# Performance work log

Hardware: AMD Instinct MI355X
Metric: run time of the kernel (lower is better)

Reference implementation:

```python
import jax, jax.numpy as jnp
import numpy as np

D_MODEL = 256
N_LAYERS = 6
PATCH = 160
N_CLASSES = 8
MAX_SEQ = 6000


def _layernorm(x, scale, bias, eps=1e-5):
    mu = jnp.mean(x, axis=-1, keepdims=True)
    var = jnp.var(x, axis=-1, keepdims=True)
    return (x - mu) * jax.lax.rsqrt(var + eps) * scale + bias


def _gru_layer(x, w_ih, w_hh, b_ih, b_hh):
    # x: [B,S,D]; w_ih,w_hh: [3D,D]; b_*: [3D]. PyTorch gate order: r,z,n.
    B, S, D = x.shape
    xp = jnp.einsum('bsd,gd->bsg', x, w_ih) + b_ih  # [B,S,3D], precompute input proj
    xp = jnp.swapaxes(xp, 0, 1)  # [S,B,3D]

    def step(h, xpt):
        gh = jnp.einsum('bd,gd->bg', h, w_hh) + b_hh
        xr, xz, xn = jnp.split(xpt, 3, axis=-1)
        hr, hz, hn = jnp.split(gh, 3, axis=-1)
        r = jax.nn.sigmoid(xr + hr)
        z = jax.nn.sigmoid(xz + hz)
        n = jnp.tanh(xn + r * hn)
        h_new = (1.0 - z) * n + z * h
        return h_new, h_new

    h0 = jnp.zeros((B, D), dtype=x.dtype)
    _, ys = jax.lax.scan(step, h0, xp)  # [S,B,D]
    return jnp.swapaxes(ys, 0, 1)


def setup_inputs() -> dict:
    key = jax.random.key(0)
    ks = jax.random.split(key, 16)
    D, L = D_MODEL, N_LAYERS
    s = lambda *sh: 0.02
    inp = {
        'waveform': jax.random.normal(ks[0], (32, 160000), dtype=jnp.float32) * 0.5,
        'conv_w': jax.random.normal(ks[1], (PATCH, D), dtype=jnp.float32) * (1.0 / np.sqrt(PATCH)),
        'pos_emb': jax.random.normal(ks[2], (MAX_SEQ, D), dtype=jnp.float32) * 0.02,
        'ln_scale': jnp.ones((L, D), dtype=jnp.float32),
        'ln_bias': jnp.zeros((L, D), dtype=jnp.float32),
        'w_ih': jax.random.normal(ks[3], (L, 3 * D, D), dtype=jnp.float32) * (1.0 / np.sqrt(D)),
        'w_hh': jax.random.normal(ks[4], (L, 3 * D, D), dtype=jnp.float32) * (1.0 / np.sqrt(D)),
        'b_ih': jnp.zeros((L, 3 * D), dtype=jnp.float32),
        'b_hh': jnp.zeros((L, 3 * D), dtype=jnp.float32),
        'fnorm_scale': jnp.ones((D,), dtype=jnp.float32),
        'fnorm_bias': jnp.zeros((D,), dtype=jnp.float32),
        'head_w1': jax.random.normal(ks[5], (D, D // 2), dtype=jnp.float32) * (1.0 / np.sqrt(D)),
        'head_b1': jnp.zeros((D // 2,), dtype=jnp.float32),
        'head_w2': jax.random.normal(ks[6], (D // 2, N_CLASSES), dtype=jnp.float32) * (1.0 / np.sqrt(D // 2)),
        'head_b2': jnp.zeros((N_CLASSES,), dtype=jnp.float32),
    }
    return inp


def reference(waveform, conv_w, pos_emb, ln_scale, ln_bias, w_ih, w_hh, b_ih, b_hh,
              fnorm_scale, fnorm_bias, head_w1, head_b1, head_w2, head_b2):
    B, T = waveform.shape
    S = T // PATCH
    # Conv1d(k=stride=PATCH, no bias) == patchify + matmul, then exact GELU
    x = waveform[:, : S * PATCH].reshape(B, S, PATCH)
    x = jax.nn.gelu(jnp.einsum('bsp,pd->bsd', x, conv_w), approximate=False)
    x = x + pos_emb[:S]
    for l in range(N_LAYERS):
        h = _layernorm(x, ln_scale[l], ln_bias[l])
        h = _gru_layer(h, w_ih[l], w_hh[l], b_ih[l], b_hh[l])
        x = x + h
    x = _layernorm(x, fnorm_scale, fnorm_bias)
    emb = jnp.mean(x, axis=1)  # [B,D]
    h = jax.nn.gelu(emb @ head_w1 + head_b1, approximate=False)  # dropout is eval no-op
    return h @ head_w2 + head_b2
```

## Files before the change

kernel.cpp:

```cpp
#include <hip/hip_runtime.h>
#include <math.h>

#define D 256
#define SEQ 1000
#define NB 32
#define PATCH 160
#define NL 6
#define M_TOTAL (NB * SEQ)
#define G3 (3 * D)
#define LDK 132

typedef _Float16 half8 __attribute__((ext_vector_type(8)));
typedef float f32x4 __attribute__((ext_vector_type(4)));

__device__ __forceinline__ float gelu_exact(float v) {
    return 0.5f * v * (1.0f + erff(v * 0.70710678118654752440f));
}

__device__ __forceinline__ void bar_lds() {
    asm volatile("s_waitcnt lgkmcnt(0)" ::: "memory");
    __builtin_amdgcn_s_barrier();
    asm volatile("" ::: "memory");
}

__device__ __forceinline__ float fast_sigmoid(float g) {
    float e = __builtin_amdgcn_exp2f(-1.44269504f * g);
    return __builtin_amdgcn_rcpf(1.f + e);
}
__device__ __forceinline__ float fast_tanh(float a) {
    a = fminf(fmaxf(a, -12.f), 12.f);
    float t = __builtin_amdgcn_exp2f(2.88539008f * a);
    return (t - 1.f) * __builtin_amdgcn_rcpf(t + 1.f);
}

__device__ __forceinline__ unsigned int pk2(float a, float b) {
    unsigned short lo = __builtin_bit_cast(unsigned short, (_Float16)a);
    unsigned short hi = __builtin_bit_cast(unsigned short, (_Float16)b);
    return (unsigned int)lo | ((unsigned int)hi << 16);
}

__global__ __launch_bounds__(256) void conv_gelu_pos(
    const float* __restrict__ wav, const float* __restrict__ cw,
    const float* __restrict__ pos, float* __restrict__ x)
{
    __shared__ float As[64][33];
    __shared__ float Bs[32][65];
    const int m0 = blockIdx.x * 64;
    const int n0 = blockIdx.y * 64;
    const int tid = threadIdx.x;
    const int tx = tid & 15;
    const int ty = tid >> 4;
    float acc[4][4] = {};

    for (int kc = 0; kc < PATCH; kc += 32) {
        for (int p = 0; p < 8; ++p) {
            int mr = p * 8 + (tid >> 5);
            int kk = tid & 31;
            int m = m0 + mr;
            int b = m / SEQ, s = m % SEQ;
            As[mr][kk] = wav[(size_t)b * 160000 + (size_t)s * PATCH + kc + kk];
        }
        for (int p = 0; p < 8; ++p) {
            int kr = p * 4 + (tid >> 6);
            int nn = tid & 63;
            Bs[kr][nn] = cw[(size_t)(kc + kr) * D + n0 + nn];
        }
        __syncthreads();
        #pragma unroll
        for (int kk = 0; kk < 32; ++kk) {
            float a[4], bb[4];
            #pragma unroll
            for (int i = 0; i < 4; ++i) a[i] = As[ty * 4 + i][kk];
            #pragma unroll
            for (int j = 0; j < 4; ++j) bb[j] = Bs[kk][tx * 4 + j];
            #pragma unroll
            for (int i = 0; i < 4; ++i)
                #pragma unroll
                for (int j = 0; j < 4; ++j)
                    acc[i][j] = fmaf(a[i], bb[j], acc[i][j]);
        }
        __syncthreads();
    }
    #pragma unroll
    for (int i = 0; i < 4; ++i) {
        int m = m0 + ty * 4 + i;
        int s = m % SEQ;
        int n = n0 + tx * 4;
        float4 v;
        v.x = gelu_exact(acc[i][0]) + pos[(size_t)s * D + n + 0];
        v.y = gelu_exact(acc[i][1]) + pos[(size_t)s * D + n + 1];
        v.z = gelu_exact(acc[i][2]) + pos[(size_t)s * D + n + 2];
        v.w = gelu_exact(acc[i][3]) + pos[(size_t)s * D + n + 3];
        *(float4*)&x[(size_t)m * D + n] = v;
    }
}

__global__ __launch_bounds__(64) void row_stats(
    const float* __restrict__ x, float* __restrict__ st)
{
    const int m = blockIdx.x;
    const int t = threadIdx.x;
    const float* r = x + (size_t)m * D;
    float s = 0.f, q = 0.f;
    #pragma unroll
    for (int i = 0; i < 4; ++i) {
        float v = r[t + 64 * i];
        s += v;
        q += v * v;
    }
    #pragma unroll
    for (int o = 32; o > 0; o >>= 1) {
        s += __shfl_down(s, o);
        q += __shfl_down(q, o);
    }
    if (t == 0) {
        float mu = s * (1.f / 256.f);
        float var = q * (1.f / 256.f) - mu * mu;
        st[2 * m]     = mu;
        st[2 * m + 1] = rsqrtf(var + 1e-5f);
    }
}

__global__ __launch_bounds__(256) void ln_xp_mfma(
    const float* __restrict__ x, const float* __restrict__ st,
    const float* __restrict__ lnsc, const float* __restrict__ lnbi,
    const float* __restrict__ wih, const float* __restrict__ bih,
    float* __restrict__ xp)
{
    __shared__ unsigned int A16[64 * LDK];
    __shared__ unsigned int B16[64 * LDK];
    __shared__ float sc_s[D], bi_s[D];
    const int m0 = blockIdx.x * 64;
    const int n0 = blockIdx.y * 64;
    const int tid = threadIdx.x;
    const int w = tid >> 6, l = tid & 63;

    sc_s[tid] = lnsc[tid];
    bi_s[tid] = lnbi[tid];
    __syncthreads();

    {
        const int r  = tid >> 2;
        const int p0 = (tid & 3) * 32;
        const int m  = m0 + r;
        const float mu = st[2 * m], rs = st[2 * m + 1];
        const float* xr = x + (size_t)m * D + 2 * p0;
        const float* wr = wih + (size_t)(n0 + r) * D + 2 * p0;
        #pragma unroll
        for (int p = 0; p < 32; p += 2) {
            const int k = 2 * (p0 + p);
            float4 v = *(const float4*)(xr + 2 * p);
            A16[r * LDK + p0 + p]     = pk2((v.x - mu) * rs * sc_s[k]     + bi_s[k],
                                            (v.y - mu) * rs * sc_s[k + 1] + bi_s[k + 1]);
            A16[r * LDK + p0 + p + 1] = pk2((v.z - mu) * rs * sc_s[k + 2] + bi_s[k + 2],
                                            (v.w - mu) * rs * sc_s[k + 3] + bi_s[k + 3]);
            float4 u = *(const float4*)(wr + 2 * p);
            B16[r * LDK + p0 + p]     = pk2(u.x, u.y);
            B16[r * LDK + p0 + p + 1] = pk2(u.z, u.w);
        }
    }
    __syncthreads();

    const int lr = l & 15, lg = l >> 4;
    uint4 afu[8];
    #pragma unroll
    for (int c = 0; c < 8; ++c)
        afu[c] = *(const uint4*)(A16 + (w * 16 + lr) * LDK + c * 16 + lg * 4);

    #pragma unroll
    for (int tile = 0; tile < 4; ++tile) {
        f32x4 acc = {0.f, 0.f, 0.f, 0.f};
        #pragma unroll
        for (int c = 0; c < 8; ++c) {
            uint4 bfu = *(const uint4*)(B16 + (tile * 16 + lr) * LDK + c * 16 + lg * 4);
            acc = __builtin_amdgcn_mfma_f32_16x16x32_f16(
                __builtin_bit_cast(half8, afu[c]),
                __builtin_bit_cast(half8, bfu), acc, 0, 0, 0);
        }
        const int col  = n0 + tile * 16 + lr;
        const int rowb = m0 + w * 16 + lg * 4;
        const float bb = bih[col];
        #pragma unroll
        for (int reg = 0; reg < 4; ++reg)
            xp[(size_t)(rowb + reg) * G3 + col] = acc[reg] + bb;
    }
}

__global__ __launch_bounds__(256) void pack_whh(
    const float* __restrict__ whh, unsigned int* __restrict__ wfrag)
{
    const int idx = blockIdx.x * 256 + threadIdx.x;
    const int j = idx & 3;
    const int l = (idx >> 2) & 63;
    const int c = (idx >> 8) & 7;
    const int t = idx >> 11;
    const int n = t * 16 + (l & 15);
    const int k = c * 32 + (l >> 4) * 8 + 2 * j;
    wfrag[idx] = pk2(whh[(size_t)n * D + k], whh[(size_t)n * D + k + 1]);
}

__global__ __launch_bounds__(512, 1) void gru_scan_mfma(
    const float* __restrict__ xp, const unsigned int* __restrict__ wfrag,
    const float* __restrict__ bhh, float* __restrict__ x)
{
    __shared__ __align__(16) unsigned int h16_lds[D / 2];
    __shared__ float gate_lds[G3];
    const int tid  = threadIdx.x;
    const int w    = tid >> 6;
    const int l    = tid & 63;
    const int d    = tid;
    const int batch = blockIdx.x;

    half8 bf[6][8];
    {
        #pragma unroll
        for (int i = 0; i < 6; ++i)
            #pragma unroll
            for (int c = 0; c < 8; ++c) {
                const uint4 v = *(const uint4*)(
                    wfrag + ((size_t)(((w * 6 + i) * 8 + c) * 64 + l)) * 4);
                bf[i][c] = __builtin_bit_cast(half8, v);
            }
    }
    float bh_r = 0.f, bh_z = 0.f, bh_n = 0.f;
    if (tid < D) {
        bh_r = bhh[d];
        bh_z = bhh[D + d];
        bh_n = bhh[2 * D + d];
    }

    const float* xpb = xp + (size_t)batch * SEQ * G3;
    float* xb = x + (size_t)batch * SEQ * D;

    float hreg = 0.f;
    if (tid < D / 2) h16_lds[tid] = 0u;
    __syncthreads();

    const int lg = l >> 4;
    for (int t = 0; t < SEQ; ++t) {
        float xr = 0.f, xz = 0.f, xn_ = 0.f, xold = 0.f;
        if (tid < D) {
            const float* xpt = xpb + (size_t)t * G3;
            xr   = xpt[d];
            xz   = xpt[D + d];
            xn_  = xpt[2 * D + d];
            xold = xb[(size_t)t * D + d];
        }

        half8 af[8];
        #pragma unroll
        for (int c = 0; c < 8; ++c)
            af[c] = __builtin_bit_cast(half8,
                *(const uint4*)(h16_lds + 16 * c + 4 * lg));

        #pragma unroll
        for (int i = 0; i < 6; ++i) {
            f32x4 cf = {0.f, 0.f, 0.f, 0.f};
            #pragma unroll
            for (int c = 0; c < 8; ++c)
                cf = __builtin_amdgcn_mfma_f32_16x16x32_f16(af[c], bf[i][c], cf, 0, 0, 0);
            if (l < 16) gate_lds[(w * 6 + i) * 16 + l] = cf[0];
        }
        bar_lds();

        if (tid < D) {
            float ar = gate_lds[d];
            float az = gate_lds[D + d];
            float an = gate_lds[2 * D + d];
            float r = fast_sigmoid(xr + ar + bh_r);
            float z = fast_sigmoid(xz + az + bh_z);
            float n = fast_tanh(xn_ + r * (an + bh_n));
            float hnew = (1.f - z) * n + z * hreg;
            hreg = hnew;
            float hn1 = __shfl_down(hnew, 1);
            if (!(d & 1)) {
                h16_lds[d >> 1] = pk2(hnew, hn1);
            }
            xb[(size_t)t * D + d] = xold + hnew;
        }
        bar_lds();
    }
}

__global__ __launch_bounds__(256) void pool_ln(
    const float* __restrict__ x, const float* __restrict__ st,
    const float* __restrict__ fsc, const float* __restrict__ fbi,
    float* __restrict__ emb)
{
    const int b = blockIdx.x;
    const int d = threadIdx.x;
    float acc = 0.f;
    for (int s = 0; s < SEQ; ++s) {
        int m = b * SEQ + s;
        acc += (x[(size_t)m * D + d] - st[2 * m]) * st[2 * m + 1];
    }
    emb[b * D + d] = (acc * (1.f / (float)SEQ)) * fsc[d] + fbi[d];
}

__global__ __launch_bounds__(256) void head_mlp(
    const float* __restrict__ emb, const float* __restrict__ w1,
    const float* __restrict__ b1, const float* __restrict__ w2,
    const float* __restrict__ b2, float* __restrict__ out)
{
    __shared__ float es[NB][D + 1];
    __shared__ float h1[NB][128 + 1];
    const int t = threadIdx.x;
    for (int i = t; i < NB * D; i += 256) es[i / D][i % D] = emb[i];
    __syncthreads();
    for (int i = t; i < NB * 128; i += 256) {
        int bb = i / 128, j = i % 128;
        float a = b1[j];
        for (int k = 0; k < D; ++k) a = fmaf(es[bb][k], w1[(size_t)k * 128 + j], a);
        h1[bb][j] = gelu_exact(a);
    }
    __syncthreads();
    for (int i = t; i < NB * 8; i += 256) {
        int bb = i / 8, c = i % 8;
        float a = b2[c];
        for (int k = 0; k < 128; ++k) a = fmaf(h1[bb][k], w2[(size_t)k * 8 + c], a);
        out[i] = a;
    }
}

extern "C" void kernel_launch(void* const* d_in, const int* in_sizes, int n_in,
                              void* d_out, int out_size, void* d_ws, size_t ws_size,
                              hipStream_t stream)
{
    const float* wav  = (const float*)d_in[0];
    const float* cw   = (const float*)d_in[1];
    const float* pos  = (const float*)d_in[2];
    const float* lnsc = (const float*)d_in[3];
    const float* lnbi = (const float*)d_in[4];
    const float* wih  = (const float*)d_in[5];
    const float* whh  = (const float*)d_in[6];
    const float* bih  = (const float*)d_in[7];
    const float* bhh  = (const float*)d_in[8];
    const float* fsc  = (const float*)d_in[9];
    const float* fbi  = (const float*)d_in[10];
    const float* hw1  = (const float*)d_in[11];
    const float* hb1  = (const float*)d_in[12];
    const float* hw2  = (const float*)d_in[13];
    const float* hb2  = (const float*)d_in[14];

    float* ws    = (float*)d_ws;
    float* x     = ws;
    float* xp    = x + (size_t)M_TOTAL * D;
    float* st    = xp + (size_t)M_TOTAL * G3;
    unsigned int* wfrag = (unsigned int*)(st + 2 * M_TOTAL);
    float* emb   = (float*)(wfrag + 98304);

    conv_gelu_pos<<<dim3(M_TOTAL / 64, D / 64), 256, 0, stream>>>(wav, cw, pos, x);

    for (int l = 0; l < NL; ++l) {
        row_stats<<<M_TOTAL, 64, 0, stream>>>(x, st);
        ln_xp_mfma<<<dim3(M_TOTAL / 64, G3 / 64), 256, 0, stream>>>(
            x, st, lnsc + (size_t)l * D, lnbi + (size_t)l * D,
            wih + (size_t)l * G3 * D, bih + (size_t)l * G3, xp);
        pack_whh<<<384, 256, 0, stream>>>(whh + (size_t)l * G3 * D, wfrag);
        gru_scan_mfma<<<NB, 512, 0, stream>>>(
            xp, wfrag, bhh + (size_t)l * G3, x);
    }

    row_stats<<<M_TOTAL, 64, 0, stream>>>(x, st);
    pool_ln<<<NB, D, 0, stream>>>(x, st, fsc, fbi, emb);
    head_mlp<<<1, 256, 0, stream>>>(emb, hw1, hb1, hw2, hb2, (float*)d_out);
}
```

Before: 7.431 ms.

## Remap GRU scan so each wave owns full gate triples, halving barriers per step

The recurrent scan kernel now assigns each wave the r, z and n gate tiles for the same 32 hidden units, so the gate nonlinearity can be computed directly from MFMA accumulators without the gate LDS exchange and its extra barrier. The hidden state is double-buffered in LDS so only one barrier per timestep is needed. The six MFMA chains are interleaved for independence. The projection kernel's load loop is also re-indexed so the four threads per row stride across the row in interleaved chunks, changing the global access pattern. This trades more idle lanes in the elementwise phase (only 16 lanes per wave active) for fewer serialization points on the latency-bound recurrence.

```diff
diff --git a/kernel.cpp b/kernel.cpp
--- a/kernel.cpp
+++ b/kernel.cpp
@@ -140,23 +140,24 @@
     __syncthreads();
 
     {
-        const int r  = tid >> 2;
-        const int p0 = (tid & 3) * 32;
-        const int m  = m0 + r;
+        const int r = tid >> 2;
+        const int q = tid & 3;
+        const int m = m0 + r;
         const float mu = st[2 * m], rs = st[2 * m + 1];
-        const float* xr = x + (size_t)m * D + 2 * p0;
-        const float* wr = wih + (size_t)(n0 + r) * D + 2 * p0;
-        #pragma unroll
-        for (int p = 0; p < 32; p += 2) {
-            const int k = 2 * (p0 + p);
-            float4 v = *(const float4*)(xr + 2 * p);
-            A16[r * LDK + p0 + p]     = pk2((v.x - mu) * rs * sc_s[k]     + bi_s[k],
-                                            (v.y - mu) * rs * sc_s[k + 1] + bi_s[k + 1]);
-            A16[r * LDK + p0 + p + 1] = pk2((v.z - mu) * rs * sc_s[k + 2] + bi_s[k + 2],
-                                            (v.w - mu) * rs * sc_s[k + 3] + bi_s[k + 3]);
-            float4 u = *(const float4*)(wr + 2 * p);
-            B16[r * LDK + p0 + p]     = pk2(u.x, u.y);
-            B16[r * LDK + p0 + p + 1] = pk2(u.z, u.w);
+        const float* xr_ = x + (size_t)m * D;
+        const float* wr_ = wih + (size_t)(n0 + r) * D;
+        #pragma unroll
+        for (int i = 0; i < 16; ++i) {
+            const int pp = 2 * q + 8 * i;
+            const int k  = 2 * pp;
+            float4 v = *(const float4*)(xr_ + k);
+            A16[r * LDK + pp]     = pk2((v.x - mu) * rs * sc_s[k]     + bi_s[k],
+                                        (v.y - mu) * rs * sc_s[k + 1] + bi_s[k + 1]);
+            A16[r * LDK + pp + 1] = pk2((v.z - mu) * rs * sc_s[k + 2] + bi_s[k + 2],
+                                        (v.w - mu) * rs * sc_s[k + 3] + bi_s[k + 3]);
+            float4 u = *(const float4*)(wr_ + k);
+            B16[r * LDK + pp]     = pk2(u.x, u.y);
+            B16[r * LDK + pp + 1] = pk2(u.z, u.w);
         }
     }
     __syncthreads();
@@ -203,80 +204,96 @@
     const float* __restrict__ xp, const unsigned int* __restrict__ wfrag,
     const float* __restrict__ bhh, float* __restrict__ x)
 {
-    __shared__ __align__(16) unsigned int h16_lds[D / 2];
-    __shared__ float gate_lds[G3];
+    __shared__ __align__(16) unsigned int h16[2][D / 2];
     const int tid  = threadIdx.x;
     const int w    = tid >> 6;
     const int l    = tid & 63;
-    const int d    = tid;
     const int batch = blockIdx.x;
 
     half8 bf[6][8];
     {
+        const int T[6] = {2 * w, 2 * w + 1, 16 + 2 * w, 17 + 2 * w,
+                          32 + 2 * w, 33 + 2 * w};
         #pragma unroll
         for (int i = 0; i < 6; ++i)
             #pragma unroll
             for (int c = 0; c < 8; ++c) {
                 const uint4 v = *(const uint4*)(
-                    wfrag + ((size_t)(((w * 6 + i) * 8 + c) * 64 + l)) * 4);
+                    wfrag + ((size_t)((T[i] * 8 + c) * 64 + l)) * 4);
                 bf[i][c] = __builtin_bit_cast(half8, v);
             }
     }
-    float bh_r = 0.f, bh_z = 0.f, bh_n = 0.f;
-    if (tid < D) {
-        bh_r = bhh[d];
-        bh_z = bhh[D + d];
-        bh_n = bhh[2 * D + d];
+    const int d0 = 32 * w + (l & 15);
+    const int d1 = d0 + 16;
+    float bh_r0 = 0.f, bh_r1 = 0.f, bh_z0 = 0.f, bh_z1 = 0.f,
+          bh_n0 = 0.f, bh_n1 = 0.f;
+    if (l < 16) {
+        bh_r0 = bhh[d0];         bh_r1 = bhh[d1];
+        bh_z0 = bhh[D + d0];     bh_z1 = bhh[D + d1];
+        bh_n0 = bhh[2 * D + d0]; bh_n1 = bhh[2 * D + d1];
     }
 
     const float* xpb = xp + (size_t)batch * SEQ * G3;
     float* xb = x + (size_t)batch * SEQ * D;
 
-    float hreg = 0.f;
-    if (tid < D / 2) h16_lds[tid] = 0u;
+    float h0 = 0.f, h1 = 0.f;
+    if (tid < D / 2) h16[0][tid] = 0u;
     __syncthreads();
 
     const int lg = l >> 4;
     for (int t = 0; t < SEQ; ++t) {
-        float xr = 0.f, xz = 0.f, xn_ = 0.f, xold = 0.f;
-        if (tid < D) {
+        const int par = t & 1;
+
+        float xr0 = 0.f, xz0 = 0.f, xn0 = 0.f, xo0 = 0.f;
+        float xr1 = 0.f, xz1 = 0.f, xn1 = 0.f, xo1 = 0.f;
+        if (l < 16) {
             const float* xpt = xpb + (size_t)t * G3;
-            xr   = xpt[d];
-            xz   = xpt[D + d];
-            xn_  = xpt[2 * D + d];
-            xold = xb[(size_t)t * D + d];
+            xr0 = xpt[d0]; xz0 = xpt[D + d0]; xn0 = xpt[2 * D + d0];
+            xr1 = xpt[d1]; xz1 = xpt[D + d1]; xn1 = xpt[2 * D + d1];
+            xo0 = xb[(size_t)t * D + d0];
+            xo1 = xb[(size_t)t * D + d1];
         }
 
         half8 af[8];
         #pragma unroll
         for (int c = 0; c < 8; ++c)
             af[c] = __builtin_bit_cast(half8,
-                *(const uint4*)(h16_lds + 16 * c + 4 * lg));
-
-        #pragma unroll
-        for (int i = 0; i < 6; ++i) {
-            f32x4 cf = {0.f, 0.f, 0.f, 0.f};
-            #pragma unroll
-            for (int c = 0; c < 8; ++c)
-                cf = __builtin_amdgcn_mfma_f32_16x16x32_f16(af[c], bf[i][c], cf, 0, 0, 0);
-            if (l < 16) gate_lds[(w * 6 + i) * 16 + l] = cf[0];
-        }
-        bar_lds();
-
-        if (tid < D) {
-            float ar = gate_lds[d];
-            float az = gate_lds[D + d];
-            float an = gate_lds[2 * D + d];
-            float r = fast_sigmoid(xr + ar + bh_r);
-            float z = fast_sigmoid(xz + az + bh_z);
-            float n = fast_tanh(xn_ + r * (an + bh_n));
-            float hnew = (1.f - z) * n + z * hreg;
-            hreg = hnew;
-            float hn1 = __shfl_down(hnew, 1);
-            if (!(d & 1)) {
-                h16_lds[d >> 1] = pk2(hnew, hn1);
+                *(const uint4*)(h16[par] + 16 * c + 4 * lg));
+
+        float g0r, g1r, g0z, g1z, g0n, g1n;
+        {
+            f32x4 c0 = {0,0,0,0}, c1 = {0,0,0,0}, c2 = {0,0,0,0},
+                  c3 = {0,0,0,0}, c4 = {0,0,0,0}, c5 = {0,0,0,0};
+            #pragma unroll
+            for (int c = 0; c < 8; ++c) {
+                c0 = __builtin_amdgcn_mfma_f32_16x16x32_f16(af[c], bf[0][c], c0, 0, 0, 0);
+                c1 = __builtin_amdgcn_mfma_f32_16x16x32_f16(af[c], bf[1][c], c1, 0, 0, 0);
+                c2 = __builtin_amdgcn_mfma_f32_16x16x32_f16(af[c], bf[2][c], c2, 0, 0, 0);
+                c3 = __builtin_amdgcn_mfma_f32_16x16x32_f16(af[c], bf[3][c], c3, 0, 0, 0);
+                c4 = __builtin_amdgcn_mfma_f32_16x16x32_f16(af[c], bf[4][c], c4, 0, 0, 0);
+                c5 = __builtin_amdgcn_mfma_f32_16x16x32_f16(af[c], bf[5][c], c5, 0, 0, 0);
             }
-            xb[(size_t)t * D + d] = xold + hnew;
+            g0r = c0[0]; g1r = c1[0]; g0z = c2[0];
+            g1z = c3[0]; g0n = c4[0]; g1n = c5[0];
+        }
+
+        if (l < 16) {
+            float r0 = fast_sigmoid(xr0 + g0r + bh_r0);
+            float r1 = fast_sigmoid(xr1 + g1r + bh_r1);
+            float z0 = fast_sigmoid(xz0 + g0z + bh_z0);
+            float z1 = fast_sigmoid(xz1 + g1z + bh_z1);
+            float n0 = fast_tanh(xn0 + r0 * (g0n + bh_n0));
+            float n1 = fast_tanh(xn1 + r1 * (g1n + bh_n1));
+            float hn0 = (1.f - z0) * n0 + z0 * h0; h0 = hn0;
+            float hn1 = (1.f - z1) * n1 + z1 * h1; h1 = hn1;
+            float hn0n = __shfl_down(hn0, 1);
+            float hn1n = __shfl_down(hn1, 1);
+            if (!(l & 1)) {
+                h16[1 - par][d0 >> 1] = pk2(hn0, hn0n);
+                h16[1 - par][d1 >> 1] = pk2(hn1, hn1n);
+            }
+            xb[(size_t)t * D + d0] = xo0 + hn0;
+            xb[(size_t)t * D + d1] = xo1 + hn1;
         }
         bar_lds();
     }
```

New measurement: 8.618 ms. +16.0%, slower.
